# Kernel tuning notes

Hardware: AMD Instinct MI355X
Metric: run time of the kernel (lower is better)

Reference implementation:

```python
import math
import jax, jax.numpy as jnp
import numpy as np

N_LAYER = 6
THETA = 2.0 ** 16
LN_EPS = 1e-5


def _ln(x):
    # LayerNorm over last dim, no affine (elementwise_affine=False)
    mu = x.mean(-1, keepdims=True)
    var = ((x - mu) ** 2).mean(-1, keepdims=True)
    return (x - mu) / jnp.sqrt(var + LN_EPS)


def _rope(phases, v):
    # phases: (T, N); v: (B, H, T, N)
    ph = (phases % 1.0) * (2.0 * math.pi)
    c, s = jnp.cos(ph), jnp.sin(ph)
    v2 = v.reshape(v.shape[:-1] + (-1, 2))
    v_rot = jnp.stack((-v2[..., 1], v2[..., 0]), axis=-1).reshape(v.shape)
    return v * c + v_rot * s


def setup_inputs() -> dict:
    key = jax.random.key(0)
    ks = jax.random.split(key, 6)
    B, T, D, nh, mult, V = 2, 512, 256, 4, 64, 256
    N = D * mult // nh  # 4096 neurons per head
    std = 0.02
    return {
        "input_ids": jax.random.randint(ks[0], (B, T), 0, V, dtype=jnp.int64),
        "embed_table": jax.random.normal(ks[1], (V, D), jnp.float32) * std,
        "encoder": jax.random.normal(ks[2], (nh, D, N), jnp.float32) * std,
        "encoder_v": jax.random.normal(ks[3], (nh, D, N), jnp.float32) * std,
        "decoder": jax.random.normal(ks[4], (nh * N, D), jnp.float32) * std,
        "lm_head": jax.random.normal(ks[5], (D, V), jnp.float32) * std,
    }


def reference(input_ids, embed_table, encoder, encoder_v, decoder, lm_head):
    B, T = input_ids.shape
    nh, D, N = encoder.shape
    # RoPE freqs: quantize(arange(N), 2) / N exponent (matches get_freqs)
    qidx = jnp.floor(jnp.arange(N, dtype=jnp.float32) / 2.0) * 2.0
    freqs = 1.0 / (THETA ** (qidx / N)) / (2.0 * math.pi)
    phases = jnp.arange(T, dtype=jnp.float32)[:, None] * freqs[None, :]  # (T, N)
    # strictly-lower causal mask (tril with diagonal=-1)
    causal = jnp.tril(jnp.ones((T, T), dtype=bool), k=-1)
    dec = decoder.reshape(nh, N, D)  # head-major, matches transpose(1,2).reshape

    x = _ln(embed_table[input_ids])[:, None]  # (B, 1, T, D)
    trace = None
    for _ in range(N_LAYER):  # shared (tied) weights across layers
        x_sparse = jax.nn.relu(jnp.einsum('bitd,hdn->bhtn', x, encoder))  # (B,H,T,N)
        qr = _rope(phases, x_sparse)
        scores = jnp.einsum('bhtn,bhsn->bhts', qr, qr)  # linear attn, no softmax
        scores = jnp.where(causal, scores, 0.0)
        ykv = _ln(jnp.einsum('bhts,bisd->bhtd', scores, x))  # (B,H,T,D)
        y_sparse = jax.nn.relu(jnp.einsum('bhtd,hdn->bhtn', ykv, encoder_v))
        xy_sparse = x_sparse * y_sparse  # elementwise gate
        trace = xy_sparse  # keep only last layer (used for neuron_trace)
        ymlp = jnp.einsum('bhtn,hnd->btd', xy_sparse, dec)[:, None]  # (B,1,T,D)
        x = _ln(x + _ln(ymlp))

    xs = x[:, 0]  # (B, T, D)
    logits = xs @ lm_head  # (B, T, V)
    embedding = xs.mean(axis=1)  # (B, D), pool_output, no mask
    neuron_trace = trace.mean(axis=2).reshape(B, -1)  # (B, H*N)
    return logits, embedding, neuron_trace
```

## Files before the change

### kernel.cpp

```cpp
#include <hip/hip_runtime.h>
#include <hip/hip_bf16.h>
#include <hip/hip_fp16.h>

#define TT 512
#define DD 256
#define NH 4
#define NN 4096
#define VV 256
#define NLAYER 6
#define BB 2
#define BH (BB * NH)
#define NPAIR 2048

typedef __attribute__((ext_vector_type(8))) short bf16x8;
typedef __attribute__((ext_vector_type(4))) float f32x4;
typedef __attribute__((ext_vector_type(8))) unsigned short us8;
typedef __attribute__((ext_vector_type(4))) unsigned short us4;

#define AS1 __attribute__((address_space(1)))
#define AS3 __attribute__((address_space(3)))

__device__ __forceinline__ void glds16(const unsigned short* g, unsigned short* l) {
  __builtin_amdgcn_global_load_lds((const AS1 void*)g, (AS3 void*)l, 16, 0, 0);
}

__device__ __forceinline__ unsigned short f2bf(float f) {
  unsigned int u = __float_as_uint(f);
  return (unsigned short)((u + 0x7FFFu + ((u >> 16) & 1u)) >> 16);
}
__device__ __forceinline__ float bf2f(unsigned short h) {
  return __uint_as_float((unsigned int)h << 16);
}
__device__ __forceinline__ float h2f(unsigned short h) {
  __half x = *reinterpret_cast<__half*>(&h);
  return __half2float(x);
}

__device__ __forceinline__ float block_sum_256(float v) {
  __shared__ float s[4];
  #pragma unroll
  for (int o = 32; o > 0; o >>= 1) v += __shfl_down(v, o);
  int lane = threadIdx.x & 63, wid = threadIdx.x >> 6;
  if (lane == 0) s[wid] = v;
  __syncthreads();
  float r = s[0] + s[1] + s[2] + s[3];
  __syncthreads();
  return r;
}

__device__ __forceinline__ float wave_sum64(float v) {
  #pragma unroll
  for (int o = 32; o > 0; o >>= 1) v += __shfl_xor(v, o);
  return v;
}

__device__ __forceinline__ void mfma_tile128_w32_dbuf(const unsigned short* __restrict__ A, int lda,
                                                      const unsigned short* __restrict__ B, int ldb,
                                                      int K, f32x4 acc[2][8],
                                                      unsigned short* As, unsigned short* Bs) {
  const int tid = threadIdx.x;
  const int lane = tid & 63, wave = tid >> 6;
  const int fm = lane & 15, fq = lane >> 4;
  const int wrow = wave << 5;
  const int lrow = lane >> 3;
  const int scol = (((lane & 7) ^ lrow) << 3);
  const unsigned short* gA = A + (size_t)(wave * 8 + lrow) * lda + scol;
  const unsigned short* gB = B + (size_t)(wave * 8 + lrow) * ldb + scol;
  const int lbase = wave * 512;
  const int swz = (fm & 7) << 4;
  #pragma unroll
  for (int i = 0; i < 4; ++i) {
    glds16(gA + (size_t)(i * 32) * lda, As + lbase + i * 2048);
    glds16(gB + (size_t)(i * 32) * ldb, Bs + lbase + i * 2048);
  }
  __syncthreads();
  int cur = 0;
  for (int k0 = 0; k0 < K; k0 += 64) {
    if (k0 + 64 < K) {
      unsigned short* nA = As + (cur ^ 1) * 8192 + lbase;
      unsigned short* nB = Bs + (cur ^ 1) * 8192 + lbase;
      #pragma unroll
      for (int i = 0; i < 4; ++i) {
        glds16(gA + (k0 + 64) + (size_t)(i * 32) * lda, nA + i * 2048);
        glds16(gB + (k0 + 64) + (size_t)(i * 32) * ldb, nB + i * 2048);
      }
    }
    const char* cA = (const char*)(As + cur * 8192);
    const char* cB = (const char*)(Bs + cur * 8192);
    #pragma unroll
    for (int kk = 0; kk < 2; ++kk) {
      bf16x8 af[2], bfv[8];
      #pragma unroll
      for (int i = 0; i < 2; ++i) {
        const int ra = wrow + i * 16 + fm;
        af[i] = *(const bf16x8*)(cA + ((((ra << 7) + (kk << 6) + (fq << 4))) ^ swz));
      }
      #pragma unroll
      for (int i = 0; i < 8; ++i) {
        const int rb = i * 16 + fm;
        bfv[i] = *(const bf16x8*)(cB + ((((rb << 7) + (kk << 6) + (fq << 4))) ^ swz));
      }
      #pragma unroll
      for (int mi = 0; mi < 2; ++mi)
        #pragma unroll
        for (int ni = 0; ni < 8; ++ni)
          acc[mi][ni] = __builtin_amdgcn_mfma_f32_16x16x32_bf16(af[mi], bfv[ni], acc[mi][ni], 0, 0, 0);
    }
    __syncthreads();
    cur ^= 1;
  }
}

__device__ __forceinline__ void mfma_tile128_dbuf(const unsigned short* __restrict__ A, int lda,
                                                  const unsigned short* __restrict__ B, int ldb,
                                                  int K, f32x4 acc[4][4],
                                                  unsigned short* As, unsigned short* Bs) {
  const int tid = threadIdx.x;
  const int lane = tid & 63, wave = tid >> 6;
  const int fm = lane & 15, fq = lane >> 4;
  const int rw = (wave >> 1) << 6, cw = (wave & 1) << 6;
  const int lrow = lane >> 3;
  const int scol = (((lane & 7) ^ lrow) << 3);
  const unsigned short* gA = A + (size_t)(wave * 8 + lrow) * lda + scol;
  const unsigned short* gB = B + (size_t)(wave * 8 + lrow) * ldb + scol;
  const int lbase = wave * 512;
  const int swz = (fm & 7) << 4;
  #pragma unroll
  for (int i = 0; i < 4; ++i) {
    glds16(gA + (size_t)(i * 32) * lda, As + lbase + i * 2048);
    glds16(gB + (size_t)(i * 32) * ldb, Bs + lbase + i * 2048);
  }
  __syncthreads();
  int cur = 0;
  for (int k0 = 0; k0 < K; k0 += 64) {
    if (k0 + 64 < K) {
      unsigned short* nA = As + (cur ^ 1) * 8192 + lbase;
      unsigned short* nB = Bs + (cur ^ 1) * 8192 + lbase;
      #pragma unroll
      for (int i = 0; i < 4; ++i) {
        glds16(gA + (k0 + 64) + (size_t)(i * 32) * lda, nA + i * 2048);
        glds16(gB + (k0 + 64) + (size_t)(i * 32) * ldb, nB + i * 2048);
      }
    }
    const char* cA = (const char*)(As + cur * 8192);
    const char* cB = (const char*)(Bs + cur * 8192);
    #pragma unroll
    for (int kk = 0; kk < 2; ++kk) {
      bf16x8 af[4], bfv[4];
      #pragma unroll
      for (int i = 0; i < 4; ++i) {
        const int ra = rw + i * 16 + fm;
        const int rb = cw + i * 16 + fm;
        af[i]  = *(const bf16x8*)(cA + ((((ra << 7) + (kk << 6) + (fq << 4))) ^ swz));
        bfv[i] = *(const bf16x8*)(cB + ((((rb << 7) + (kk << 6) + (fq << 4))) ^ swz));
      }
      #pragma unroll
      for (int mi = 0; mi < 4; ++mi)
        #pragma unroll
        for (int ni = 0; ni < 4; ++ni)
          acc[mi][ni] = __builtin_amdgcn_mfma_f32_16x16x32_bf16(af[mi], bfv[ni], acc[mi][ni], 0, 0, 0);
    }
    __syncthreads();
    cur ^= 1;
  }
}


__global__ __launch_bounds__(256) void k_csinit(unsigned int* __restrict__ cs) {
  int idx = blockIdx.x * 256 + threadIdx.x;
  int t = idx >> 11, p = idx & (NPAIR - 1);
  const float INV2PI = 0.15915494309189535f;
  const float TWOPI = 6.283185307179586f;
  float f = exp2f(-16.0f * (float)(2 * p) / (float)NN) * INV2PI;
  float ph = fmodf((float)t * f, 1.0f) * TWOPI;
  float s, c;
  sincosf(ph, &s, &c);
  __half hc = __float2half_rn(c), hs = __float2half_rn(s);
  unsigned short uc = *reinterpret_cast<unsigned short*>(&hc);
  unsigned short us_ = *reinterpret_cast<unsigned short*>(&hs);
  cs[idx] = ((unsigned int)us_ << 16) | uc;
}

__global__ __launch_bounds__(256) void k_tcast(const float* __restrict__ in,
                                               unsigned short* __restrict__ out,
                                               int R, int C) {
  __shared__ float tile[64][65];
  const size_t zoff = (size_t)blockIdx.z * R * C;
  const int r0 = blockIdx.y * 64, c0 = blockIdx.x * 64;
  const int cl = threadIdx.x & 63, r4 = threadIdx.x >> 6;
  #pragma unroll 4
  for (int i = 0; i < 16; ++i) {
    int rl = r4 * 16 + i;
    tile[rl][cl] = in[zoff + (size_t)(r0 + rl) * C + c0 + cl];
  }
  __syncthreads();
  #pragma unroll 4
  for (int i = 0; i < 16; ++i) {
    int ccl = r4 * 16 + i;
    out[zoff + (size_t)(c0 + ccl) * R + r0 + cl] = f2bf(tile[cl][ccl]);
  }
}

__global__ __launch_bounds__(256) void k_embed_ln(const int* __restrict__ idw,
                                                  const float* __restrict__ tbl,
                                                  float* __restrict__ x,
                                                  unsigned short* __restrict__ xbf,
                                                  unsigned short* __restrict__ xTbf) {
  __shared__ int s_id;
  int row = blockIdx.x, tid = threadIdx.x;
  if (tid == 0) {
    bool is64 = true;
    for (int i = 1; i < 64; i += 2)
      if (idw[i] != 0) { is64 = false; break; }
    s_id = is64 ? idw[2 * row] : idw[row];
  }
  __syncthreads();
  int id = s_id;
  float v = tbl[(size_t)id * DD + tid];
  float mu = block_sum_256(v) * (1.0f / DD);
  float d = v - mu;
  float var = block_sum_256(d * d) * (1.0f / DD);
  float r = d * rsqrtf(var + 1e-5f);
  x[(size_t)row * DD + tid] = r;
  unsigned short rb = f2bf(r);
  xbf[(size_t)row * DD + tid] = rb;
  int b = row >> 9, t = row & 511;
  xTbf[((size_t)b * DD + tid) * TT + t] = rb;
}


__global__ __launch_bounds__(256) void k_enc(const unsigned short* __restrict__ xbf,
                                             const unsigned short* __restrict__ encT,
                                             const unsigned int* __restrict__ csh,
                                             unsigned short* __restrict__ xsp,
                                             unsigned short* __restrict__ qr) {
  __shared__ unsigned short smem[32768];
  unsigned short* As = smem;
  unsigned short* Bs = smem + 16384;
  float* smemf = (float*)smem;
  const int tid = threadIdx.x;
  const int lin = blockIdx.x;
  const int bh = lin & 7, r0 = lin >> 3;
  const int b = bh >> 2, h = bh & 3;
  const int m0 = (r0 >> 5) * 128, n0 = (r0 & 31) * 128;
  f32x4 acc[2][8] = {};
  mfma_tile128_w32_dbuf(xbf + (size_t)b * TT * DD + (size_t)m0 * DD, DD,
                        encT + (size_t)h * NN * DD + (size_t)n0 * DD, DD, DD, acc, As, Bs);
  const int lane = tid & 63, wave = tid >> 6;
  const int fm = lane & 15, fq = lane >> 4;
  float* Scw = smemf + wave * (16 * 132);
  const int rr4 = lane >> 4, c0 = (lane & 15) << 3;
  const size_t base = (size_t)bh * TT * NN;
  #pragma unroll
  for (int mi = 0; mi < 2; ++mi) {
    if (mi) asm volatile("s_waitcnt lgkmcnt(0)" ::: "memory");
    #pragma unroll
    for (int ni = 0; ni < 8; ++ni)
      #pragma unroll
      for (int r = 0; r < 4; ++r)
        Scw[(fq * 4 + r) * 132 + ni * 16 + fm] = acc[mi][ni][r];
    asm volatile("s_waitcnt lgkmcnt(0)" ::: "memory");
    #pragma unroll
    for (int k = 0; k < 4; ++k) {
      const int rr = k * 4 + rr4;
      float v[8];
      *(float4*)&v[0] = *(const float4*)&Scw[rr * 132 + c0];
      *(float4*)&v[4] = *(const float4*)&Scw[rr * 132 + c0 + 4];
      const int t = m0 + wave * 32 + mi * 16 + rr;
      const int n = n0 + c0;
      #pragma unroll
      for (int j = 0; j < 8; ++j) v[j] = fmaxf(v[j], 0.0f);
      us8 o;
      #pragma unroll
      for (int j = 0; j < 8; ++j) o[j] = f2bf(v[j]);
      size_t off = base + (size_t)t * NN + n;
      *(us8*)(xsp + off) = o;
      const unsigned short* cp = (const unsigned short*)(csh + (size_t)t * NPAIR + (n >> 1));
      us8 cv = *(const us8*)cp;
      us8 q;
      #pragma unroll
      for (int j = 0; j < 4; ++j) {
        float c = h2f(cv[2 * j]), s = h2f(cv[2 * j + 1]);
        float ve = v[2 * j], vo = v[2 * j + 1];
        q[2 * j]     = f2bf(ve * c - vo * s);
        q[2 * j + 1] = f2bf(vo * c + ve * s);
      }
      *(us8*)(qr + off) = q;
    }
  }
}

__global__ __launch_bounds__(256) void k_scores_part(const unsigned short* __restrict__ qr,
                                                     float* __restrict__ scp) {
  __shared__ float smemf[16384];
  unsigned short* As = (unsigned short*)smemf;
  unsigned short* Bs = As + 16384;
  const int lin = blockIdx.x;
  const int xcd = lin & 7, slot = lin >> 3;
  const int zg = slot / 10, p = slot - zg * 10;
  const int z = xcd * 4 + zg;
  const int bh = z >> 2, kc = z & 3;
  const int mt = (p > 0) + (p > 2) + (p > 5);
  const int nt = p - mt * (mt + 1) / 2;
  const int m0 = mt * 128, n0 = nt * 128;
  const unsigned short* Q = qr + (size_t)bh * TT * NN + kc * 1024;
  f32x4 acc[4][4] = {};
  mfma_tile128_dbuf(Q + (size_t)m0 * NN, NN, Q + (size_t)n0 * NN, NN, 1024, acc, As, Bs);
  const int lane = threadIdx.x & 63, wave = threadIdx.x >> 6;
  const int fm = lane & 15, fq = lane >> 4;
  const int rw = (wave >> 1) << 6, cw = (wave & 1) << 6;
  float* C = scp + (size_t)z * TT * TT;
  const bool diag = (m0 == n0);
  #pragma unroll
  for (int ni = 0; ni < 4; ++ni) {
    int s = n0 + cw + ni * 16 + fm;
    #pragma unroll
    for (int mi = 0; mi < 4; ++mi) {
      int trow = m0 + rw + mi * 16 + (fq << 2);
      #pragma unroll
      for (int r = 0; r < 4; ++r) {
        float v = acc[mi][ni][r];
        if (diag && s >= trow + r) v = 0.0f;
        C[(size_t)(trow + r) * TT + s] = v;
      }
    }
  }
}

__global__ __launch_bounds__(256) void k_ykv_part(const float* __restrict__ scp,
                                                  const unsigned short* __restrict__ xTbf,
                                                  float* __restrict__ ykvp) {
  __shared__ unsigned short As[64][40];
  __shared__ unsigned short Bs[256][40];
  const int tid = threadIdx.x;
  const int lin = blockIdx.x;
  const int bh = lin & 7, r0 = lin >> 3;
  const int m0 = (r0 & 7) * 64, ks = r0 >> 3, b = bh >> 2;
  if (ks * 128 >= m0 + 64) return;
  float* C = ykvp + ((size_t)(bh * 4 + ks) * TT + m0) * DD;
  const int lane = tid & 63, wave = tid >> 6;
  const int srow = tid >> 2, sk = (tid & 3) << 3;
  const int fm = lane & 15, fq = lane >> 4;
  const int t = m0 + srow;
  const size_t abase0 = (size_t)(bh * 4) * TT * TT + (size_t)t * TT;
  const unsigned short* Brow = xTbf + ((size_t)b * DD + tid) * TT + ks * 128;
  f32x4 acc[16] = {};
  for (int k0 = 0; k0 < 128; k0 += 32) {
    const int s0 = ks * 128 + k0 + sk;
    const float* p = scp + abase0 + s0;
    float sum[8];
    float4 u0 = *(const float4*)(p);
    float4 u1 = *(const float4*)(p + 4);
    sum[0] = u0.x; sum[1] = u0.y; sum[2] = u0.z; sum[3] = u0.w;
    sum[4] = u1.x; sum[5] = u1.y; sum[6] = u1.z; sum[7] = u1.w;
    #pragma unroll
    for (int kc = 1; kc < 4; ++kc) {
      float4 v0 = *(const float4*)(p + (size_t)kc * TT * TT);
      float4 v1 = *(const float4*)(p + (size_t)kc * TT * TT + 4);
      sum[0] += v0.x; sum[1] += v0.y; sum[2] += v0.z; sum[3] += v0.w;
      sum[4] += v1.x; sum[5] += v1.y; sum[6] += v1.z; sum[7] += v1.w;
    }
    us8 av;
    #pragma unroll
    for (int j = 0; j < 8; ++j) av[j] = f2bf(sum[j]);
    us8 bv0 = *(const us8*)(Brow + k0);
    us8 bv1 = *(const us8*)(Brow + k0 + 8);
    us8 bv2 = *(const us8*)(Brow + k0 + 16);
    us8 bv3 = *(const us8*)(Brow + k0 + 24);
    __syncthreads();
    *(us8*)(&As[srow][sk]) = av;
    *(us8*)(&Bs[tid][0]) = bv0;
    *(us8*)(&Bs[tid][8]) = bv1;
    *(us8*)(&Bs[tid][16]) = bv2;
    *(us8*)(&Bs[tid][24]) = bv3;
    __syncthreads();
    bf16x8 a = *(const bf16x8*)(&As[wave * 16 + fm][fq << 3]);
    #pragma unroll
    for (int ni = 0; ni < 16; ++ni) {
      bf16x8 bfr = *(const bf16x8*)(&Bs[ni * 16 + fm][fq << 3]);
      acc[ni] = __builtin_amdgcn_mfma_f32_16x16x32_bf16(a, bfr, acc[ni], 0, 0, 0);
    }
  }
  const int trow = wave * 16 + (fq << 2);
  #pragma unroll
  for (int ni = 0; ni < 16; ++ni)
    #pragma unroll
    for (int r = 0; r < 4; ++r)
      C[(size_t)(trow + r) * DD + ni * 16 + fm] = acc[ni][r];
}

__global__ __launch_bounds__(256) void k_ykv_red(const float* __restrict__ ykvp,
                                                 unsigned short* __restrict__ ykvbf) {
  int row = blockIdx.x * 4 + (threadIdx.x >> 6);
  int lane = threadIdx.x & 63;
  int bh = row >> 9, t = row & 511;
  int d0 = lane << 2;
  int nks = (t >> 7) + 1;
  size_t base = ((size_t)(bh * 4) * TT + t) * DD + d0;
  f32x4 v = *(const f32x4*)(ykvp + base);
  if (nks > 1) v += *(const f32x4*)(ykvp + base + (size_t)TT * DD);
  if (nks > 2) v += *(const f32x4*)(ykvp + base + (size_t)2 * TT * DD);
  if (nks > 3) v += *(const f32x4*)(ykvp + base + (size_t)3 * TT * DD);
  float mu = wave_sum64(v.x + v.y + v.z + v.w) * (1.0f / DD);
  f32x4 d = v - mu;
  float var = wave_sum64(d.x * d.x + d.y * d.y + d.z * d.z + d.w * d.w) * (1.0f / DD);
  f32x4 r = d * rsqrtf(var + 1e-5f);
  us4 rb;
  #pragma unroll
  for (int j = 0; j < 4; ++j) rb[j] = f2bf(r[j]);
  *(us4*)(ykvbf + (size_t)row * DD + d0) = rb;
}

__global__ __launch_bounds__(256) void k_ysp_xy(const unsigned short* __restrict__ ykvbf,
                                                const unsigned short* __restrict__ encvT,
                                                const unsigned short* __restrict__ xsp,
                                                unsigned short* __restrict__ xy) {
  __shared__ unsigned short smem[32768];
  unsigned short* As = smem;
  unsigned short* Bs = smem + 16384;
  float* smemf = (float*)smem;
  const int tid = threadIdx.x;
  const int lin = blockIdx.x;
  const int bh = lin & 7, r0 = lin >> 3;
  const int h = bh & 3;
  const int m0 = (r0 >> 5) * 128, n0 = (r0 & 31) * 128;
  f32x4 acc[2][8] = {};
  mfma_tile128_w32_dbuf(ykvbf + (size_t)bh * TT * DD + (size_t)m0 * DD, DD,
                        encvT + (size_t)h * NN * DD + (size_t)n0 * DD, DD, DD, acc, As, Bs);
  const int lane = tid & 63, wave = tid >> 6;
  const int fm = lane & 15, fq = lane >> 4;
  float* Scw = smemf + wave * (16 * 132);
  const int rr4 = lane >> 4, c0 = (lane & 15) << 3;
  const size_t base = (size_t)bh * TT * NN;
  #pragma unroll
  for (int mi = 0; mi < 2; ++mi) {
    if (mi) asm volatile("s_waitcnt lgkmcnt(0)" ::: "memory");
    #pragma unroll
    for (int ni = 0; ni < 8; ++ni)
      #pragma unroll
      for (int r = 0; r < 4; ++r)
        Scw[(fq * 4 + r) * 132 + ni * 16 + fm] = acc[mi][ni][r];
    asm volatile("s_waitcnt lgkmcnt(0)" ::: "memory");
    #pragma unroll
    for (int k = 0; k < 4; ++k) {
      const int rr = k * 4 + rr4;
      float v[8];
      *(float4*)&v[0] = *(const float4*)&Scw[rr * 132 + c0];
      *(float4*)&v[4] = *(const float4*)&Scw[rr * 132 + c0 + 4];
      const int t = m0 + wave * 32 + mi * 16 + rr;
      const int n = n0 + c0;
      size_t off = base + (size_t)t * NN + n;
      us8 x0 = *(const us8*)(xsp + off);
      us8 o;
      #pragma unroll
      for (int j = 0; j < 8; ++j)
        o[j] = f2bf(bf2f(x0[j]) * fmaxf(v[j], 0.0f));
      *(us8*)(xy + off) = o;
    }
  }
}

__global__ __launch_bounds__(256) void k_ymlp(const unsigned short* __restrict__ xy,
                                              const unsigned short* __restrict__ decT,
                                              float* __restrict__ ym32) {
  __shared__ float smemf[16384];
  unsigned short* As = (unsigned short*)smemf;
  unsigned short* Bs = As + 16384;
  const int lin = blockIdx.x;
  const int xcd = lin & 7, r0 = lin >> 3;
  const int z = xcd * 8 + (r0 >> 3);
  const int tile = r0 & 7;
  const int bh = z >> 3, ks = z & 7, h = bh & 3;
  const int m0 = (tile & 3) * 128, n0 = (tile >> 2) * 128;
  f32x4 acc[4][4] = {};
  mfma_tile128_dbuf(xy + (size_t)bh * TT * NN + (size_t)m0 * NN + ks * 512, NN,
                    decT + (size_t)h * DD * NN + (size_t)n0 * NN + ks * 512, NN,
                    512, acc, As, Bs);
  const int lane = threadIdx.x & 63, wave = threadIdx.x >> 6;
  const int fm = lane & 15, fq = lane >> 4;
  const int rw = (wave >> 1) << 6, cw = (wave & 1) << 6;
  float* C = ym32 + (size_t)z * TT * DD;
  #pragma unroll
  for (int ni = 0; ni < 4; ++ni) {
    int d = n0 + cw + ni * 16 + fm;
    #pragma unroll
    for (int mi = 0; mi < 4; ++mi) {
      int trow = m0 + rw + mi * 16 + (fq << 2);
      #pragma unroll
      for (int r = 0; r < 4; ++r)
        C[(size_t)(trow + r) * DD + d] = acc[mi][ni][r];
    }
  }
}

__global__ __launch_bounds__(256) void k_ln2(float* __restrict__ x,
                                             const float* __restrict__ ym32,
                                             unsigned short* __restrict__ xbf,
                                             unsigned short* __restrict__ xTbf) {
  int row = blockIdx.x * 4 + (threadIdx.x >> 6);
  int lane = threadIdx.x & 63;
  int b = row >> 9, t = row & 511;
  int d0 = lane << 2;
  f32x4 y = {0.0f, 0.0f, 0.0f, 0.0f};
  size_t rbase = (size_t)t * DD + d0;
  #pragma unroll
  for (int p = 0; p < 32; ++p)
    y += *(const f32x4*)(ym32 + (size_t)(b * 32 + p) * TT * DD + rbase);
  float mu = wave_sum64(y.x + y.y + y.z + y.w) * (1.0f / DD);
  f32x4 d = y - mu;
  float var = wave_sum64(d.x * d.x + d.y * d.y + d.z * d.z + d.w * d.w) * (1.0f / DD);
  f32x4 ly = d * rsqrtf(var + 1e-5f);
  f32x4 xv = *(const f32x4*)(x + (size_t)row * DD + d0) + ly;
  float mu2 = wave_sum64(xv.x + xv.y + xv.z + xv.w) * (1.0f / DD);
  f32x4 d2 = xv - mu2;
  float var2 = wave_sum64(d2.x * d2.x + d2.y * d2.y + d2.z * d2.z + d2.w * d2.w) * (1.0f / DD);
  f32x4 r = d2 * rsqrtf(var2 + 1e-5f);
  *(f32x4*)(x + (size_t)row * DD + d0) = r;
  us4 rb;
  #pragma unroll
  for (int j = 0; j < 4; ++j) rb[j] = f2bf(r[j]);
  *(us4*)(xbf + (size_t)row * DD + d0) = rb;
  #pragma unroll
  for (int j = 0; j < 4; ++j)
    xTbf[((size_t)b * DD + d0 + j) * TT + t] = rb[j];
}

__global__ __launch_bounds__(256) void k_trace_part(const unsigned short* __restrict__ xy,
                                                    float* __restrict__ part) {
  const int lin = blockIdx.x;
  const int ts = lin & 15, nc = (lin >> 4) & 1, bh = lin >> 5;
  const int n0 = nc * 2048 + threadIdx.x * 8;
  const size_t base = (size_t)bh * TT * NN + n0;
  float acc[8];
  #pragma unroll
  for (int j = 0; j < 8; ++j) acc[j] = 0.0f;
  for (int t = ts * 32; t < ts * 32 + 32; ++t) {
    us8 v = *(const us8*)(xy + base + (size_t)t * NN);
    #pragma unroll
    for (int j = 0; j < 8; ++j) acc[j] += bf2f(v[j]);
  }
  float* o = part + (size_t)(bh * 16 + ts) * NN + n0;
  #pragma unroll
  for (int j = 0; j < 8; ++j) o[j] = acc[j];
}

__global__ __launch_bounds__(256) void k_trace_red(const float* __restrict__ part,
                                                   float* __restrict__ out) {
  int idx = blockIdx.x * 256 + threadIdx.x;
  int bh = idx >> 12, n = idx & 4095;
  float s = 0.0f;
  #pragma unroll
  for (int ts = 0; ts < 16; ++ts)
    s += part[(size_t)(bh * 16 + ts) * NN + n];
  out[idx] = s * (1.0f / TT);
}

__global__ __launch_bounds__(256) void k_logits(const float* __restrict__ x,
                                                const float* __restrict__ W,
                                                float* __restrict__ out) {
  __shared__ float xs[DD];
  int row = blockIdx.x, tid = threadIdx.x;
  xs[tid] = x[(size_t)row * DD + tid];
  __syncthreads();
  float s = 0.0f;
  #pragma unroll 8
  for (int d = 0; d < DD; ++d) s = fmaf(xs[d], W[(size_t)d * VV + tid], s);
  out[(size_t)row * VV + tid] = s;
}

__global__ __launch_bounds__(256) void k_embed_part(const float* __restrict__ x,
                                                    float* __restrict__ part) {
  const int lin = blockIdx.x;
  const int tc = lin & 31, b = lin >> 5;
  const int d = threadIdx.x;
  float s = 0.0f;
  #pragma unroll
  for (int i = 0; i < 16; ++i)
    s += x[(size_t)(b * TT + tc * 16 + i) * DD + d];
  part[(size_t)lin * DD + d] = s;
}

__global__ __launch_bounds__(256) void k_embed_red(const float* __restrict__ part,
                                                   float* __restrict__ out) {
  int idx = blockIdx.x * 256 + threadIdx.x;
  int b = idx >> 8, d = idx & 255;
  float s = 0.0f;
  #pragma unroll
  for (int tc = 0; tc < 32; ++tc)
    s += part[(size_t)(b * 32 + tc) * DD + d];
  out[idx] = s * (1.0f / TT);
}

extern "C" void kernel_launch(void* const* d_in, const int* in_sizes, int n_in,
                              void* d_out, int out_size, void* d_ws, size_t ws_size,
                              hipStream_t stream) {
  const int*   ids  = (const int*)d_in[0];
  const float* tbl  = (const float*)d_in[1];
  const float* enc  = (const float*)d_in[2];
  const float* encv = (const float*)d_in[3];
  const float* dec  = (const float*)d_in[4];
  const float* lmh  = (const float*)d_in[5];

  float* ws   = (float*)d_ws;
  float* x    = ws;
  unsigned short* ykvbf = (unsigned short*)(x + 262144);
  float* ym32 = (float*)(ykvbf + 1048576);
  unsigned short* xbf   = (unsigned short*)(ym32 + 8388608);
  unsigned short* xTbf  = xbf + 262144;
  unsigned short* encT  = xTbf + 262144;
  unsigned short* encvT = encT + 4194304;
  unsigned short* decT  = encvT + 4194304;
  unsigned short* xspbf = decT + 4194304;
  unsigned short* qxybf = xspbf + 16777216;
  unsigned int* cs = (unsigned int*)(qxybf + 16777216);
  float* scp  = (float*)(cs + 2097152);
  float* ykvp = scp + 8388608;
  float* tpart = scp;
  float* epart = scp + 524288;

  float* out_logits = (float*)d_out;
  float* out_embed  = out_logits + (size_t)BB * TT * VV;
  float* out_trace  = out_embed + (size_t)BB * DD;

  k_csinit<<<(TT * NPAIR) / 256, 256, 0, stream>>>(cs);
  k_tcast<<<dim3(NN / 64, DD / 64, NH), 256, 0, stream>>>(enc,  encT,  DD, NN);
  k_tcast<<<dim3(NN / 64, DD / 64, NH), 256, 0, stream>>>(encv, encvT, DD, NN);
  k_tcast<<<dim3(DD / 64, NN / 64, NH), 256, 0, stream>>>(dec,  decT,  NN, DD);

  k_embed_ln<<<BB * TT, 256, 0, stream>>>(ids, tbl, x, xbf, xTbf);
  for (int l = 0; l < NLAYER; ++l) {
    k_enc        <<<1024, 256, 0, stream>>>(xbf, encT, cs, xspbf, qxybf);
    k_scores_part<<<320, 256, 0, stream>>>(qxybf, scp);
    k_ykv_part   <<<256, 256, 0, stream>>>(scp, xTbf, ykvp);
    k_ykv_red    <<<BH * TT / 4, 256, 0, stream>>>(ykvp, ykvbf);
    k_ysp_xy     <<<1024, 256, 0, stream>>>(ykvbf, encvT, xspbf, qxybf);
    k_ymlp       <<<512, 256, 0, stream>>>(qxybf, decT, ym32);
    k_ln2        <<<BB * TT / 4, 256, 0, stream>>>(x, ym32, xbf, xTbf);
  }
  k_trace_part<<<256, 256, 0, stream>>>(qxybf, tpart);
  k_trace_red <<<128, 256, 0, stream>>>(tpart, out_trace);
  k_logits    <<<BB * TT, 256, 0, stream>>>(x, lmh, out_logits);
  k_embed_part<<<64, 256, 0, stream>>>(x, epart);
  k_embed_red <<<2, 256, 0, stream>>>(epart, out_embed);
}
```

Before: 721.3 us.

## Halve ymlp split-K factor and merge three weight transpose-cast launches

The decoder GEMM now splits K into 4 chunks of 1024 instead of 8 chunks of 512. That halves the grid to 256 blocks and halves the fp32 partial buffers that k_ln2 must write and read back. The block-to-work mapping is also changed so the low bits pick bh. Separately, the three one-time weight transpose/cast launches are merged into a single kernel to save launch overhead. The trade-off is fewer blocks on the GPU, which lowers occupancy and parallelism for the ymlp GEMM.

```diff
diff --git a/kernel.cpp b/kernel.cpp
--- a/kernel.cpp
+++ b/kernel.cpp
@@ -181,12 +181,29 @@
   cs[idx] = ((unsigned int)us_ << 16) | uc;
 }
 
-__global__ __launch_bounds__(256) void k_tcast(const float* __restrict__ in,
-                                               unsigned short* __restrict__ out,
-                                               int R, int C) {
+__global__ __launch_bounds__(256) void k_tcast3(const float* __restrict__ enc,
+                                                const float* __restrict__ encv,
+                                                const float* __restrict__ dec,
+                                                unsigned short* __restrict__ encT,
+                                                unsigned short* __restrict__ encvT,
+                                                unsigned short* __restrict__ decT) {
   __shared__ float tile[64][65];
-  const size_t zoff = (size_t)blockIdx.z * R * C;
-  const int r0 = blockIdx.y * 64, c0 = blockIdx.x * 64;
+  const int lin = blockIdx.x;
+  const float* in;
+  unsigned short* out;
+  int R, C, bx, by, bz;
+  if (lin < 2048) {
+    const int which = lin >> 10;
+    in = which ? encv : enc; out = which ? encvT : encT; R = DD; C = NN;
+    const int r = lin & 1023;
+    bx = r & 63; by = (r >> 6) & 3; bz = r >> 8;
+  } else {
+    in = dec; out = decT; R = NN; C = DD;
+    const int r = lin - 2048;
+    bx = r & 3; by = (r >> 2) & 63; bz = r >> 8;
+  }
+  const size_t zoff = (size_t)bz * R * C;
+  const int r0 = by * 64, c0 = bx * 64;
   const int cl = threadIdx.x & 63, r4 = threadIdx.x >> 6;
   #pragma unroll 4
   for (int i = 0; i < 16; ++i) {
@@ -467,15 +484,14 @@
   unsigned short* As = (unsigned short*)smemf;
   unsigned short* Bs = As + 16384;
   const int lin = blockIdx.x;
-  const int xcd = lin & 7, r0 = lin >> 3;
-  const int z = xcd * 8 + (r0 >> 3);
-  const int tile = r0 & 7;
-  const int bh = z >> 3, ks = z & 7, h = bh & 3;
+  const int bh = lin & 7, r0 = lin >> 3;
+  const int ks = r0 >> 3, tile = r0 & 7;
+  const int z = bh * 4 + ks, h = bh & 3;
   const int m0 = (tile & 3) * 128, n0 = (tile >> 2) * 128;
   f32x4 acc[4][4] = {};
-  mfma_tile128_dbuf(xy + (size_t)bh * TT * NN + (size_t)m0 * NN + ks * 512, NN,
-                    decT + (size_t)h * DD * NN + (size_t)n0 * NN + ks * 512, NN,
-                    512, acc, As, Bs);
+  mfma_tile128_dbuf(xy + (size_t)bh * TT * NN + (size_t)m0 * NN + ks * 1024, NN,
+                    decT + (size_t)h * DD * NN + (size_t)n0 * NN + ks * 1024, NN,
+                    1024, acc, As, Bs);
   const int lane = threadIdx.x & 63, wave = threadIdx.x >> 6;
   const int fm = lane & 15, fq = lane >> 4;
   const int rw = (wave >> 1) << 6, cw = (wave & 1) << 6;
@@ -504,8 +520,8 @@
   f32x4 y = {0.0f, 0.0f, 0.0f, 0.0f};
   size_t rbase = (size_t)t * DD + d0;
   #pragma unroll
-  for (int p = 0; p < 32; ++p)
-    y += *(const f32x4*)(ym32 + (size_t)(b * 32 + p) * TT * DD + rbase);
+  for (int p = 0; p < 16; ++p)
+    y += *(const f32x4*)(ym32 + (size_t)(b * 16 + p) * TT * DD + rbase);
   float mu = wave_sum64(y.x + y.y + y.z + y.w) * (1.0f / DD);
   f32x4 d = y - mu;
   float var = wave_sum64(d.x * d.x + d.y * d.y + d.z * d.z + d.w * d.w) * (1.0f / DD);
@@ -623,9 +639,7 @@
   float* out_trace  = out_embed + (size_t)BB * DD;
 
   k_csinit<<<(TT * NPAIR) / 256, 256, 0, stream>>>(cs);
-  k_tcast<<<dim3(NN / 64, DD / 64, NH), 256, 0, stream>>>(enc,  encT,  DD, NN);
-  k_tcast<<<dim3(NN / 64, DD / 64, NH), 256, 0, stream>>>(encv, encvT, DD, NN);
-  k_tcast<<<dim3(DD / 64, NN / 64, NH), 256, 0, stream>>>(dec,  decT,  NN, DD);
+  k_tcast3<<<3072, 256, 0, stream>>>(enc, encv, dec, encT, encvT, decT);
 
   k_embed_ln<<<BB * TT, 256, 0, stream>>>(ids, tbl, x, xbf, xTbf);
   for (int l = 0; l < NLAYER; ++l) {
@@ -634,7 +648,7 @@
     k_ykv_part   <<<256, 256, 0, stream>>>(scp, xTbf, ykvp);
     k_ykv_red    <<<BH * TT / 4, 256, 0, stream>>>(ykvp, ykvbf);
     k_ysp_xy     <<<1024, 256, 0, stream>>>(ykvbf, encvT, xspbf, qxybf);
-    k_ymlp       <<<512, 256, 0, stream>>>(qxybf, decT, ym32);
+    k_ymlp       <<<256, 256, 0, stream>>>(qxybf, decT, ym32);
     k_ln2        <<<BB * TT / 4, 256, 0, stream>>>(x, ym32, xbf, xTbf);
   }
   k_trace_part<<<256, 256, 0, stream>>>(qxybf, tpart);
```

New measurement: 704.7 us. -2.3%, faster.
